# Optimization experiments

Hardware: AMD Instinct MI355X
Metric: run time of the kernel (lower is better)

The kernel has to match this reference:

```python
import jax, jax.numpy as jnp
import numpy as np
import math

B, L, C = 1, 4096, 1024
H = 16
D = C // H  # head_dim = 64


def setup_inputs() -> dict:
    key = jax.random.key(0)
    ks = jax.random.split(key, 5)
    s = 1.0 / math.sqrt(C)
    return {
        "x": jax.random.normal(ks[0], (B, L, C), dtype=jnp.float32),
        "Wq": jax.random.normal(ks[1], (C, C), dtype=jnp.float32) * s,
        "Wk": jax.random.normal(ks[2], (C, C), dtype=jnp.float32) * s,
        "Wv": jax.random.normal(ks[3], (C, C), dtype=jnp.float32) * s,
        "Wo": jax.random.normal(ks[4], (C, C), dtype=jnp.float32) * s,
    }


def reference(x, Wq, Wk, Wv, Wo):
    # Projections (bias=False). Wq etc. are applied as x @ W (equivalent
    # parameterization to torch Linear's x @ W.T with transposed storage).
    q = (x @ Wq).reshape(B, L, H, D).transpose(0, 2, 1, 3)  # (B,H,L,D)
    k = (x @ Wk).reshape(B, L, H, D).transpose(0, 2, 1, 3)
    v = (x @ Wv).reshape(B, L, H, D).transpose(0, 2, 1, 3)

    scale = 1.0 / math.sqrt(D)
    scores = jnp.einsum("bhqd,bhkd->bhqk", q, k) * scale  # (B,H,L,L)
    causal = jnp.tril(jnp.ones((L, L), dtype=bool))
    scores = jnp.where(causal[None, None, :, :], scores, -jnp.inf)
    probs = jax.nn.softmax(scores, axis=-1)  # dropout p=0 -> identity

    out = jnp.einsum("bhqk,bhkd->bhqd", probs, v)  # (B,H,L,D)
    out = out.transpose(0, 2, 1, 3).reshape(B, L, C)
    return out @ Wo  # resid dropout p=0 -> identity
```

## Files before the change

### kernel.cpp

```cpp
#include <hip/hip_runtime.h>

#define L_SEQ 4096
#define C_DIM 1024
#define H_NUM 16
#define D_HEAD 64
#define LDQKV 3072

typedef __bf16 bf16x8 __attribute__((ext_vector_type(8)));
typedef __bf16 bf16x4 __attribute__((ext_vector_type(4)));
typedef float f32x4 __attribute__((ext_vector_type(4)));
typedef float f32x16 __attribute__((ext_vector_type(16)));
typedef unsigned int u32;
typedef u32 u32x4 __attribute__((ext_vector_type(4)));

#define AS1 __attribute__((address_space(1)))
#define AS3 __attribute__((address_space(3)))

#define SC_LOG2E 0.1803368801111204f

__device__ inline __bf16 f2bf(float f) {
  unsigned u = __builtin_bit_cast(unsigned, f);
  u = (u + 0x7fffu + ((u >> 16) & 1u)) >> 16;
  unsigned short s = (unsigned short)u;
  return __builtin_bit_cast(__bf16, s);
}

__device__ inline void gload_lds16(const __bf16* g, __bf16* l) {
  __builtin_amdgcn_global_load_lds((const AS1 void*)g, (AS3 void*)l, 16, 0, 0);
}

__global__ __launch_bounds__(256) void cvt_f32_bf16(const float* __restrict__ in,
                                                    __bf16* __restrict__ out) {
  int i = (blockIdx.x * 256 + threadIdx.x) * 4;
  float4 v = *(const float4*)(in + i);
  bf16x4 o = {f2bf(v.x), f2bf(v.y), f2bf(v.z), f2bf(v.w)};
  *(bf16x4*)(out + i) = o;
}

__global__ __launch_bounds__(256) void transpose_cvt4(const float* __restrict__ W0,
                                                      const float* __restrict__ W1,
                                                      const float* __restrict__ W2,
                                                      const float* __restrict__ W3,
                                                      __bf16* __restrict__ dst) {
  __shared__ float t[32][33];
  const int z = blockIdx.z;
  const float* W = (z == 0) ? W0 : (z == 1) ? W1 : (z == 2) ? W2 : W3;
  __bf16* Wt = dst + (size_t)z * 1048576;
  const int tx = threadIdx.x, ty = threadIdx.y;
  const int c0 = blockIdx.x * 32, r0 = blockIdx.y * 32;
#pragma unroll
  for (int k = 0; k < 4; ++k)
    t[ty + k * 8][tx] = W[(size_t)(r0 + ty + k * 8) * C_DIM + c0 + tx];
  __syncthreads();
#pragma unroll
  for (int k = 0; k < 4; ++k)
    Wt[(size_t)(c0 + ty + k * 8) * C_DIM + r0 + tx] = f2bf(t[tx][ty + k * 8]);
}

__global__ __launch_bounds__(256) void transpose_v(const __bf16* __restrict__ QKV,
                                                   __bf16* __restrict__ Vt) {
  __shared__ __bf16 t[32][34];
  const int tx = threadIdx.x, ty = threadIdx.y;
  const int q0 = blockIdx.x * 32, c0 = blockIdx.y * 32;
#pragma unroll
  for (int k = 0; k < 4; ++k)
    t[ty + k * 8][tx] = QKV[(size_t)(q0 + ty + k * 8) * LDQKV + 2048 + c0 + tx];
  __syncthreads();
#pragma unroll
  for (int k = 0; k < 4; ++k)
    Vt[(size_t)(c0 + ty + k * 8) * L_SEQ + q0 + tx] = t[tx][ty + k * 8];
}

template <bool OUT_BF16>
__global__ __launch_bounds__(256) void gemm_bt(const __bf16* __restrict__ A,
                                               const __bf16* __restrict__ Bt,
                                               void* __restrict__ Cp,
                                               int M, int N, int K,
                                               float cscale, int scale_ncols) {
  __shared__ __bf16 As[128 * 32];
  __shared__ __bf16 Bs[128 * 32];
  const int tid = threadIdx.x;
  const int lane = tid & 63;
  const int wave = tid >> 6;
  const int wm = wave >> 1, wn = wave & 1;
  const int c16 = lane & 15, g4 = lane >> 4;
  const int srow = lane >> 2, scol = (lane & 3) * 8;

  f32x4 acc[4][4] = {};

  const size_t arow0 = (size_t)blockIdx.x * 128;
  const size_t brow0 = (size_t)blockIdx.y * 128;

  for (int kt = 0; kt < K; kt += 32) {
#pragma unroll
    for (int i = 0; i < 2; ++i) {
      const int row = i * 64 + wave * 16 + srow;
      gload_lds16(A + (arow0 + row) * K + kt + scol, As + (i * 64 + wave * 16) * 32);
      gload_lds16(Bt + (brow0 + row) * K + kt + scol, Bs + (i * 64 + wave * 16) * 32);
    }
    __syncthreads();
    bf16x8 af[4], bfr[4];
#pragma unroll
    for (int mi = 0; mi < 4; ++mi)
      af[mi] = *(const bf16x8*)(As + (wm * 64 + mi * 16 + c16) * 32 + g4 * 8);
#pragma unroll
    for (int ni = 0; ni < 4; ++ni)
      bfr[ni] = *(const bf16x8*)(Bs + (wn * 64 + ni * 16 + c16) * 32 + g4 * 8);
#pragma unroll
    for (int mi = 0; mi < 4; ++mi)
#pragma unroll
      for (int ni = 0; ni < 4; ++ni)
        acc[mi][ni] = __builtin_amdgcn_mfma_f32_16x16x32_bf16(af[mi], bfr[ni], acc[mi][ni], 0, 0, 0);
    __syncthreads();
  }

  const float esc = ((int)brow0 < scale_ncols) ? cscale : 1.0f;
#pragma unroll
  for (int mi = 0; mi < 4; ++mi)
#pragma unroll
    for (int ni = 0; ni < 4; ++ni)
#pragma unroll
      for (int i = 0; i < 4; ++i) {
        size_t row = arow0 + wm * 64 + mi * 16 + g4 * 4 + i;
        size_t col = brow0 + wn * 64 + ni * 16 + c16;
        if (OUT_BF16)
          ((__bf16*)Cp)[row * N + col] = f2bf(acc[mi][ni][i] * esc);
        else
          ((float*)Cp)[row * N + col] = acc[mi][ni][i];
      }
}

__global__ __launch_bounds__(256, 2) void attn_fwd(const __bf16* __restrict__ Q,
                                                   const __bf16* __restrict__ Kg,
                                                   const __bf16* __restrict__ Vt,
                                                   __bf16* __restrict__ O) {
  const int bid = blockIdx.x;
  const int h = bid & 15;
  const int qt = 31 - (bid >> 4);
  const int nt = 2 * qt + 2;

  __shared__ __bf16 Ks[2][64 * 64];
  __shared__ __bf16 Vs[2][64 * 64];

  const int tid = threadIdx.x;
  const int lane = tid & 63;
  const int wave = tid >> 6;
  const int l31 = lane & 31;
  const int hl = lane >> 5;
  const int qbase = qt * 128 + wave * 32;
  const int q = qbase + l31;
  const int kvmax_w = (qbase + 31) >> 6;

  const int rl = lane >> 3;
  const int cs = (lane & 7) ^ rl;

  auto stage = [&](int kv, int b) {
#pragma unroll
    for (int i = 0; i < 2; ++i) {
      const int r = (i * 4 + wave) * 8 + rl;
      gload_lds16(Kg + (size_t)(kv * 64 + r) * LDQKV + h * D_HEAD + cs * 8,
                  &Ks[b][(i * 4 + wave) * 512]);
      gload_lds16(Vt + (size_t)(h * D_HEAD + r) * L_SEQ + kv * 64 + cs * 8,
                  &Vs[b][(i * 4 + wave) * 512]);
    }
  };

  stage(0, 0);

  bf16x8 qf[4];
  {
    const __bf16* qp = Q + (size_t)q * LDQKV + h * D_HEAD + hl * 8;
#pragma unroll
    for (int s = 0; s < 4; ++s) qf[s] = *(const bf16x8*)(qp + s * 16);
  }

  f32x16 acc0 = {}, acc1 = {};
  float m = -1e30f, lsum = 0.f;

  int cur = 0;
  for (int kv = 0; kv < nt; ++kv) {
    if (kv + 1 < nt) {
      stage(kv + 1, cur ^ 1);
      asm volatile("s_waitcnt vmcnt(4)" ::: "memory");
    } else {
      asm volatile("s_waitcnt vmcnt(0)" ::: "memory");
    }
    __builtin_amdgcn_sched_barrier(0);
    __builtin_amdgcn_s_barrier();
    __builtin_amdgcn_sched_barrier(0);

    if (kv <= kvmax_w) {
      char* const KsB = (char*)&Ks[cur][0];
      char* const VsB = (char*)&Vs[cur][0];

      f32x16 st0 = {}, st1 = {};
      __builtin_amdgcn_s_setprio(1);
#pragma unroll
      for (int s = 0; s < 4; ++s) {
        const int ch = s * 2 + hl;
        bf16x8 a0 = *(const bf16x8*)(KsB + l31 * 128 + ((ch ^ (l31 & 7)) << 4));
        bf16x8 a1 = *(const bf16x8*)(KsB + (32 + l31) * 128 + ((ch ^ (l31 & 7)) << 4));
        st0 = __builtin_amdgcn_mfma_f32_32x32x16_bf16(a0, qf[s], st0, 0, 0, 0);
        st1 = __builtin_amdgcn_mfma_f32_32x32x16_bf16(a1, qf[s], st1, 0, 0, 0);
      }
      __builtin_amdgcn_s_setprio(0);

      if (kv == kvmax_w) {
#pragma unroll
        for (int r = 0; r < 16; ++r) {
          const int kr = (r & 3) + 8 * (r >> 2) + 4 * hl;
          const int k0 = kv * 64 + kr;
          st0[r] = (k0 <= q) ? st0[r] : -1e30f;
          st1[r] = (k0 + 32 <= q) ? st1[r] : -1e30f;
        }
      }

      float t[16];
#pragma unroll
      for (int r = 0; r < 16; ++r) t[r] = fmaxf(st0[r], st1[r]);
#pragma unroll
      for (int w = 8; w > 0; w >>= 1)
#pragma unroll
        for (int r = 0; r < w; ++r) t[r] = fmaxf(t[r], t[r + w]);
      float mx = fmaxf(t[0], __shfl_xor(t[0], 32, 64));
      const float mnew = fmaxf(m, mx);
      const float corr = exp2f(m - mnew);
      m = mnew;

#pragma unroll
      for (int r = 0; r < 16; ++r) {
        st0[r] = exp2f(st0[r] - m);
        st1[r] = exp2f(st1[r] - m);
      }
      float sm[16];
#pragma unroll
      for (int r = 0; r < 16; ++r) sm[r] = st0[r] + st1[r];
#pragma unroll
      for (int w = 8; w > 0; w >>= 1)
#pragma unroll
        for (int r = 0; r < w; ++r) sm[r] = sm[r] + sm[r + w];
      float sl = sm[0] + __shfl_xor(sm[0], 32, 64);
      lsum = lsum * corr + sl;
      acc0 *= corr;
      acc1 *= corr;

      u32 w0[8], w1[8];
#pragma unroll
      for (int i = 0; i < 8; ++i) {
        asm("v_cvt_pk_bf16_f32 %0, %1, %2" : "=v"(w0[i]) : "v"(st0[2 * i]), "v"(st0[2 * i + 1]));
        asm("v_cvt_pk_bf16_f32 %0, %1, %2" : "=v"(w1[i]) : "v"(st1[2 * i]), "v"(st1[2 * i + 1]));
      }
      u32 e0a = (u32)__shfl_xor((int)(hl ? w0[0] : w0[2]), 32, 64);
      u32 e0b = (u32)__shfl_xor((int)(hl ? w0[1] : w0[3]), 32, 64);
      u32 e0c = (u32)__shfl_xor((int)(hl ? w0[4] : w0[6]), 32, 64);
      u32 e0d = (u32)__shfl_xor((int)(hl ? w0[5] : w0[7]), 32, 64);
      u32 e1a = (u32)__shfl_xor((int)(hl ? w1[0] : w1[2]), 32, 64);
      u32 e1b = (u32)__shfl_xor((int)(hl ? w1[1] : w1[3]), 32, 64);
      u32 e1c = (u32)__shfl_xor((int)(hl ? w1[4] : w1[6]), 32, 64);
      u32 e1d = (u32)__shfl_xor((int)(hl ? w1[5] : w1[7]), 32, 64);
      u32x4 f0 = hl ? (u32x4){e0a, e0b, w0[2], w0[3]} : (u32x4){w0[0], w0[1], e0a, e0b};
      u32x4 f1 = hl ? (u32x4){e0c, e0d, w0[6], w0[7]} : (u32x4){w0[4], w0[5], e0c, e0d};
      u32x4 f2 = hl ? (u32x4){e1a, e1b, w1[2], w1[3]} : (u32x4){w1[0], w1[1], e1a, e1b};
      u32x4 f3 = hl ? (u32x4){e1c, e1d, w1[6], w1[7]} : (u32x4){w1[4], w1[5], e1c, e1d};
      bf16x8 pb0 = __builtin_bit_cast(bf16x8, f0);
      bf16x8 pb1 = __builtin_bit_cast(bf16x8, f1);
      bf16x8 pb2 = __builtin_bit_cast(bf16x8, f2);
      bf16x8 pb3 = __builtin_bit_cast(bf16x8, f3);

      __builtin_amdgcn_s_setprio(1);
#pragma unroll
      for (int s = 0; s < 4; ++s) {
        const bf16x8 pb = (s == 0) ? pb0 : (s == 1) ? pb1 : (s == 2) ? pb2 : pb3;
        const int ch = s * 2 + hl;
        bf16x8 va0 = *(const bf16x8*)(VsB + l31 * 128 + ((ch ^ (l31 & 7)) << 4));
        bf16x8 va1 = *(const bf16x8*)(VsB + (32 + l31) * 128 + ((ch ^ (l31 & 7)) << 4));
        acc0 = __builtin_amdgcn_mfma_f32_32x32x16_bf16(va0, pb, acc0, 0, 0, 0);
        acc1 = __builtin_amdgcn_mfma_f32_32x32x16_bf16(va1, pb, acc1, 0, 0, 0);
      }
      __builtin_amdgcn_s_setprio(0);
    }

    __builtin_amdgcn_sched_barrier(0);
    __builtin_amdgcn_s_barrier();
    __builtin_amdgcn_sched_barrier(0);
    cur ^= 1;
  }

  const float rinv = 1.0f / lsum;
  char* const Po = (char*)&Ks[0][0] + wave * 4096;
#pragma unroll
  for (int dt = 0; dt < 2; ++dt) {
#pragma unroll
    for (int i = 0; i < 8; ++i) {
      const int r = 2 * i;
      const int d = dt * 32 + (r & 3) + 8 * (r >> 2) + 4 * hl;
      float lo = (dt ? acc1[r] : acc0[r]) * rinv;
      float hi = (dt ? acc1[r + 1] : acc0[r + 1]) * rinv;
      u32 wv;
      asm("v_cvt_pk_bf16_f32 %0, %1, %2" : "=v"(wv) : "v"(lo), "v"(hi));
      *(u32*)(Po + l31 * 128 + (((d >> 3) ^ (l31 & 7)) << 4) + (d & 7) * 2) = wv;
    }
  }
  asm volatile("s_waitcnt lgkmcnt(0)" ::: "memory");
  __builtin_amdgcn_sched_barrier(0);
#pragma unroll
  for (int j = 0; j < 4; ++j) {
    const int qr = lane >> 1;
    const int c = (lane & 1) * 4 + j;
    bf16x8 ov = *(const bf16x8*)(Po + qr * 128 + ((c ^ (qr & 7)) << 4));
    *(bf16x8*)(O + (size_t)(qbase + qr) * C_DIM + h * D_HEAD + c * 8) = ov;
  }
}

extern "C" void kernel_launch(void* const* d_in, const int* in_sizes, int n_in,
                              void* d_out, int out_size, void* d_ws, size_t ws_size,
                              hipStream_t stream) {
  const float* x = (const float*)d_in[0];
  const float* Wq = (const float*)d_in[1];
  const float* Wk = (const float*)d_in[2];
  const float* Wv = (const float*)d_in[3];
  const float* Wo = (const float*)d_in[4];
  float* out = (float*)d_out;

  char* ws = (char*)d_ws;
  __bf16* xb    = (__bf16*)(ws);
  __bf16* WqkvT = (__bf16*)(ws + (8u << 20));
  __bf16* QKVb  = (__bf16*)(ws + (16u << 20));
  __bf16* Vtb   = (__bf16*)(ws + (40u << 20));
  __bf16* WoT   = WqkvT + (size_t)3 * 1048576;
  __bf16* Ab    = xb;

  cvt_f32_bf16<<<4096, 256, 0, stream>>>(x, xb);

  transpose_cvt4<<<dim3(32, 32, 4), dim3(32, 8), 0, stream>>>(Wq, Wk, Wv, Wo, WqkvT);

  gemm_bt<true><<<dim3(L_SEQ / 128, LDQKV / 128), 256, 0, stream>>>(
      xb, WqkvT, QKVb, L_SEQ, LDQKV, C_DIM, SC_LOG2E, 1024);

  transpose_v<<<dim3(L_SEQ / 32, C_DIM / 32), dim3(32, 8), 0, stream>>>(QKVb, Vtb);

  attn_fwd<<<512, 256, 0, stream>>>(QKVb, QKVb + 1024, Vtb, Ab);

  gemm_bt<false><<<dim3(L_SEQ / 128, C_DIM / 128), 256, 0, stream>>>(
      Ab, WoT, out, L_SEQ, C_DIM, C_DIM, 1.0f, 0);
}
```

Before: 258.6 us.

## Pair complementary causal query tiles per block for balanced attention work

The attention kernel now gives each block two 64-row query tiles, p and 63-p, processed back to back so every block runs exactly 65 KV iterations. This replaces 128-row tiles with uneven causal work and per-wave idle iterations, removing load imbalance and wasted barrier trips. Blocks shrink to 128 threads (2 waves), each wave staging more loads, and a separate LDS buffer holds the first tile's epilogue output. The risk is lower per-block parallelism and more K/V traffic, since each 64-row tile reloads K/V independently.

```diff
diff --git a/kernel.cpp b/kernel.cpp
--- a/kernel.cpp
+++ b/kernel.cpp
@@ -130,58 +130,86 @@
       }
 }
 
-__global__ __launch_bounds__(256, 2) void attn_fwd(const __bf16* __restrict__ Q,
+__global__ __launch_bounds__(128, 2) void attn_fwd(const __bf16* __restrict__ Q,
                                                    const __bf16* __restrict__ Kg,
                                                    const __bf16* __restrict__ Vt,
                                                    __bf16* __restrict__ O) {
   const int bid = blockIdx.x;
   const int h = bid & 15;
-  const int qt = 31 - (bid >> 4);
-  const int nt = 2 * qt + 2;
+  const int p = bid >> 4;
+  const int nA = 64 - p;
+  const int NT = 65;
 
   __shared__ __bf16 Ks[2][64 * 64];
   __shared__ __bf16 Vs[2][64 * 64];
+  __shared__ __bf16 PoS[2][2048];
 
   const int tid = threadIdx.x;
   const int lane = tid & 63;
   const int wave = tid >> 6;
   const int l31 = lane & 31;
   const int hl = lane >> 5;
-  const int qbase = qt * 128 + wave * 32;
-  const int q = qbase + l31;
-  const int kvmax_w = (qbase + 31) >> 6;
-
   const int rl = lane >> 3;
   const int cs = (lane & 7) ^ rl;
+  const int thr = wave * 32 + l31;
 
   auto stage = [&](int kv, int b) {
 #pragma unroll
-    for (int i = 0; i < 2; ++i) {
-      const int r = (i * 4 + wave) * 8 + rl;
+    for (int i = 0; i < 4; ++i) {
+      const int r = (i * 2 + wave) * 8 + rl;
       gload_lds16(Kg + (size_t)(kv * 64 + r) * LDQKV + h * D_HEAD + cs * 8,
-                  &Ks[b][(i * 4 + wave) * 512]);
+                  &Ks[b][(i * 2 + wave) * 512]);
       gload_lds16(Vt + (size_t)(h * D_HEAD + r) * L_SEQ + kv * 64 + cs * 8,
-                  &Vs[b][(i * 4 + wave) * 512]);
+                  &Vs[b][(i * 2 + wave) * 512]);
     }
   };
 
   stage(0, 0);
 
+  int qbase = (nA - 1) * 64 + wave * 32;
   bf16x8 qf[4];
   {
-    const __bf16* qp = Q + (size_t)q * LDQKV + h * D_HEAD + hl * 8;
+    const __bf16* qp = Q + (size_t)(qbase + l31) * LDQKV + h * D_HEAD + hl * 8;
 #pragma unroll
     for (int s = 0; s < 4; ++s) qf[s] = *(const bf16x8*)(qp + s * 16);
   }
 
   f32x16 acc0 = {}, acc1 = {};
   float m = -1e30f, lsum = 0.f;
-
   int cur = 0;
-  for (int kv = 0; kv < nt; ++kv) {
-    if (kv + 1 < nt) {
-      stage(kv + 1, cur ^ 1);
-      asm volatile("s_waitcnt vmcnt(4)" ::: "memory");
+
+  auto epilogue = [&](int qb) {
+    const float rinv = 1.0f / lsum;
+    char* const Po = (char*)&PoS[wave][0];
+#pragma unroll
+    for (int dt = 0; dt < 2; ++dt) {
+#pragma unroll
+      for (int i = 0; i < 8; ++i) {
+        const int r = 2 * i;
+        const int d = dt * 32 + (r & 3) + 8 * (r >> 2) + 4 * hl;
+        float lo = (dt ? acc1[r] : acc0[r]) * rinv;
+        float hi = (dt ? acc1[r + 1] : acc0[r + 1]) * rinv;
+        u32 wv;
+        asm("v_cvt_pk_bf16_f32 %0, %1, %2" : "=v"(wv) : "v"(lo), "v"(hi));
+        *(u32*)(Po + l31 * 128 + (((d >> 3) ^ (l31 & 7)) << 4) + (d & 7) * 2) = wv;
+      }
+    }
+    asm volatile("s_waitcnt lgkmcnt(0)" ::: "memory");
+    __builtin_amdgcn_sched_barrier(0);
+#pragma unroll
+    for (int j = 0; j < 4; ++j) {
+      const int qr = lane >> 1;
+      const int c = (lane & 1) * 4 + j;
+      bf16x8 ov = *(const bf16x8*)(Po + qr * 128 + ((c ^ (qr & 7)) << 4));
+      *(bf16x8*)(O + (size_t)(qb + qr) * C_DIM + h * D_HEAD + c * 8) = ov;
+    }
+  };
+
+  for (int it = 0; it < NT; ++it) {
+    if (it + 1 < NT) {
+      const int kvn = (it + 1 < nA) ? it + 1 : it + 1 - nA;
+      stage(kvn, cur ^ 1);
+      asm volatile("s_waitcnt vmcnt(8)" ::: "memory");
     } else {
       asm volatile("s_waitcnt vmcnt(0)" ::: "memory");
     }
@@ -189,127 +217,114 @@
     __builtin_amdgcn_s_barrier();
     __builtin_amdgcn_sched_barrier(0);
 
-    if (kv <= kvmax_w) {
-      char* const KsB = (char*)&Ks[cur][0];
-      char* const VsB = (char*)&Vs[cur][0];
-
-      f32x16 st0 = {}, st1 = {};
-      __builtin_amdgcn_s_setprio(1);
-#pragma unroll
-      for (int s = 0; s < 4; ++s) {
-        const int ch = s * 2 + hl;
-        bf16x8 a0 = *(const bf16x8*)(KsB + l31 * 128 + ((ch ^ (l31 & 7)) << 4));
-        bf16x8 a1 = *(const bf16x8*)(KsB + (32 + l31) * 128 + ((ch ^ (l31 & 7)) << 4));
-        st0 = __builtin_amdgcn_mfma_f32_32x32x16_bf16(a0, qf[s], st0, 0, 0, 0);
-        st1 = __builtin_amdgcn_mfma_f32_32x32x16_bf16(a1, qf[s], st1, 0, 0, 0);
+    char* const KsB = (char*)&Ks[cur][0];
+    char* const VsB = (char*)&Vs[cur][0];
+    const bool diag = (it == nA - 1) || (it == NT - 1);
+
+    f32x16 st0 = {}, st1 = {};
+    __builtin_amdgcn_s_setprio(1);
+#pragma unroll
+    for (int s = 0; s < 4; ++s) {
+      const int ch = s * 2 + hl;
+      bf16x8 a0 = *(const bf16x8*)(KsB + l31 * 128 + ((ch ^ (l31 & 7)) << 4));
+      bf16x8 a1 = *(const bf16x8*)(KsB + (32 + l31) * 128 + ((ch ^ (l31 & 7)) << 4));
+      st0 = __builtin_amdgcn_mfma_f32_32x32x16_bf16(a0, qf[s], st0, 0, 0, 0);
+      st1 = __builtin_amdgcn_mfma_f32_32x32x16_bf16(a1, qf[s], st1, 0, 0, 0);
+    }
+    __builtin_amdgcn_s_setprio(0);
+
+    if (diag) {
+#pragma unroll
+      for (int r = 0; r < 16; ++r) {
+        const int kr = (r & 3) + 8 * (r >> 2) + 4 * hl;
+        st0[r] = (kr <= thr) ? st0[r] : -1e30f;
+        st1[r] = (kr + 32 <= thr) ? st1[r] : -1e30f;
       }
-      __builtin_amdgcn_s_setprio(0);
-
-      if (kv == kvmax_w) {
-#pragma unroll
-        for (int r = 0; r < 16; ++r) {
-          const int kr = (r & 3) + 8 * (r >> 2) + 4 * hl;
-          const int k0 = kv * 64 + kr;
-          st0[r] = (k0 <= q) ? st0[r] : -1e30f;
-          st1[r] = (k0 + 32 <= q) ? st1[r] : -1e30f;
-        }
-      }
-
-      float t[16];
-#pragma unroll
-      for (int r = 0; r < 16; ++r) t[r] = fmaxf(st0[r], st1[r]);
-#pragma unroll
-      for (int w = 8; w > 0; w >>= 1)
-#pragma unroll
-        for (int r = 0; r < w; ++r) t[r] = fmaxf(t[r], t[r + w]);
-      float mx = fmaxf(t[0], __shfl_xor(t[0], 32, 64));
-      const float mnew = fmaxf(m, mx);
-      const float corr = exp2f(m - mnew);
-      m = mnew;
-
-#pragma unroll
-      for (int r = 0; r < 16; ++r) {
-        st0[r] = exp2f(st0[r] - m);
-        st1[r] = exp2f(st1[r] - m);
-      }
-      float sm[16];
-#pragma unroll
-      for (int r = 0; r < 16; ++r) sm[r] = st0[r] + st1[r];
-#pragma unroll
-      for (int w = 8; w > 0; w >>= 1)
-#pragma unroll
-        for (int r = 0; r < w; ++r) sm[r] = sm[r] + sm[r + w];
-      float sl = sm[0] + __shfl_xor(sm[0], 32, 64);
-      lsum = lsum * corr + sl;
-      acc0 *= corr;
-      acc1 *= corr;
-
-      u32 w0[8], w1[8];
-#pragma unroll
-      for (int i = 0; i < 8; ++i) {
-        asm("v_cvt_pk_bf16_f32 %0, %1, %2" : "=v"(w0[i]) : "v"(st0[2 * i]), "v"(st0[2 * i + 1]));
-        asm("v_cvt_pk_bf16_f32 %0, %1, %2" : "=v"(w1[i]) : "v"(st1[2 * i]), "v"(st1[2 * i + 1]));
-      }
-      u32 e0a = (u32)__shfl_xor((int)(hl ? w0[0] : w0[2]), 32, 64);
-      u32 e0b = (u32)__shfl_xor((int)(hl ? w0[1] : w0[3]), 32, 64);
-      u32 e0c = (u32)__shfl_xor((int)(hl ? w0[4] : w0[6]), 32, 64);
-      u32 e0d = (u32)__shfl_xor((int)(hl ? w0[5] : w0[7]), 32, 64);
-      u32 e1a = (u32)__shfl_xor((int)(hl ? w1[0] : w1[2]), 32, 64);
-      u32 e1b = (u32)__shfl_xor((int)(hl ? w1[1] : w1[3]), 32, 64);
-      u32 e1c = (u32)__shfl_xor((int)(hl ? w1[4] : w1[6]), 32, 64);
-      u32 e1d = (u32)__shfl_xor((int)(hl ? w1[5] : w1[7]), 32, 64);
-      u32x4 f0 = hl ? (u32x4){e0a, e0b, w0[2], w0[3]} : (u32x4){w0[0], w0[1], e0a, e0b};
-      u32x4 f1 = hl ? (u32x4){e0c, e0d, w0[6], w0[7]} : (u32x4){w0[4], w0[5], e0c, e0d};
-      u32x4 f2 = hl ? (u32x4){e1a, e1b, w1[2], w1[3]} : (u32x4){w1[0], w1[1], e1a, e1b};
-      u32x4 f3 = hl ? (u32x4){e1c, e1d, w1[6], w1[7]} : (u32x4){w1[4], w1[5], e1c, e1d};
-      bf16x8 pb0 = __builtin_bit_cast(bf16x8, f0);
-      bf16x8 pb1 = __builtin_bit_cast(bf16x8, f1);
-      bf16x8 pb2 = __builtin_bit_cast(bf16x8, f2);
-      bf16x8 pb3 = __builtin_bit_cast(bf16x8, f3);
-
-      __builtin_amdgcn_s_setprio(1);
-#pragma unroll
-      for (int s = 0; s < 4; ++s) {
-        const bf16x8 pb = (s == 0) ? pb0 : (s == 1) ? pb1 : (s == 2) ? pb2 : pb3;
-        const int ch = s * 2 + hl;
-        bf16x8 va0 = *(const bf16x8*)(VsB + l31 * 128 + ((ch ^ (l31 & 7)) << 4));
-        bf16x8 va1 = *(const bf16x8*)(VsB + (32 + l31) * 128 + ((ch ^ (l31 & 7)) << 4));
-        acc0 = __builtin_amdgcn_mfma_f32_32x32x16_bf16(va0, pb, acc0, 0, 0, 0);
-        acc1 = __builtin_amdgcn_mfma_f32_32x32x16_bf16(va1, pb, acc1, 0, 0, 0);
-      }
-      __builtin_amdgcn_s_setprio(0);
-    }
+    }
+
+    float t[16];
+#pragma unroll
+    for (int r = 0; r < 16; ++r) t[r] = fmaxf(st0[r], st1[r]);
+#pragma unroll
+    for (int w = 8; w > 0; w >>= 1)
+#pragma unroll
+      for (int r = 0; r < w; ++r) t[r] = fmaxf(t[r], t[r + w]);
+    float mx = fmaxf(t[0], __shfl_xor(t[0], 32, 64));
+    const float mnew = fmaxf(m, mx);
+    const float corr = exp2f(m - mnew);
+    m = mnew;
+
+#pragma unroll
+    for (int r = 0; r < 16; ++r) {
+      st0[r] = exp2f(st0[r] - m);
+      st1[r] = exp2f(st1[r] - m);
+    }
+    float sm[16];
+#pragma unroll
+    for (int r = 0; r < 16; ++r) sm[r] = st0[r] + st1[r];
+#pragma unroll
+    for (int w = 8; w > 0; w >>= 1)
+#pragma unroll
+      for (int r = 0; r < w; ++r) sm[r] = sm[r] + sm[r + w];
+    float sl = sm[0] + __shfl_xor(sm[0], 32, 64);
+    lsum = lsum * corr + sl;
+    acc0 *= corr;
+    acc1 *= corr;
+
+    u32 w0[8], w1[8];
+#pragma unroll
+    for (int i = 0; i < 8; ++i) {
+      asm("v_cvt_pk_bf16_f32 %0, %1, %2" : "=v"(w0[i]) : "v"(st0[2 * i]), "v"(st0[2 * i + 1]));
+      asm("v_cvt_pk_bf16_f32 %0, %1, %2" : "=v"(w1[i]) : "v"(st1[2 * i]), "v"(st1[2 * i + 1]));
+    }
+    u32 e0a = (u32)__shfl_xor((int)(hl ? w0[0] : w0[2]), 32, 64);
+    u32 e0b = (u32)__shfl_xor((int)(hl ? w0[1] : w0[3]), 32, 64);
+    u32 e0c = (u32)__shfl_xor((int)(hl ? w0[4] : w0[6]), 32, 64);
+    u32 e0d = (u32)__shfl_xor((int)(hl ? w0[5] : w0[7]), 32, 64);
+    u32 e1a = (u32)__shfl_xor((int)(hl ? w1[0] : w1[2]), 32, 64);
+    u32 e1b = (u32)__shfl_xor((int)(hl ? w1[1] : w1[3]), 32, 64);
+    u32 e1c = (u32)__shfl_xor((int)(hl ? w1[4] : w1[6]), 32, 64);
+    u32 e1d = (u32)__shfl_xor((int)(hl ? w1[5] : w1[7]), 32, 64);
+    u32x4 f0 = hl ? (u32x4){e0a, e0b, w0[2], w0[3]} : (u32x4){w0[0], w0[1], e0a, e0b};
+    u32x4 f1 = hl ? (u32x4){e0c, e0d, w0[6], w0[7]} : (u32x4){w0[4], w0[5], e0c, e0d};
+    u32x4 f2 = hl ? (u32x4){e1a, e1b, w1[2], w1[3]} : (u32x4){w1[0], w1[1], e1a, e1b};
+    u32x4 f3 = hl ? (u32x4){e1c, e1d, w1[6], w1[7]} : (u32x4){w1[4], w1[5], e1c, e1d};
+    bf16x8 pb0 = __builtin_bit_cast(bf16x8, f0);
+    bf16x8 pb1 = __builtin_bit_cast(bf16x8, f1);
+    bf16x8 pb2 = __builtin_bit_cast(bf16x8, f2);
+    bf16x8 pb3 = __builtin_bit_cast(bf16x8, f3);
+
+    __builtin_amdgcn_s_setprio(1);
+#pragma unroll
+    for (int s = 0; s < 4; ++s) {
+      const bf16x8 pb = (s == 0) ? pb0 : (s == 1) ? pb1 : (s == 2) ? pb2 : pb3;
+      const int ch = s * 2 + hl;
+      bf16x8 va0 = *(const bf16x8*)(VsB + l31 * 128 + ((ch ^ (l31 & 7)) << 4));
+      bf16x8 va1 = *(const bf16x8*)(VsB + (32 + l31) * 128 + ((ch ^ (l31 & 7)) << 4));
+      acc0 = __builtin_amdgcn_mfma_f32_32x32x16_bf16(va0, pb, acc0, 0, 0, 0);
+      acc1 = __builtin_amdgcn_mfma_f32_32x32x16_bf16(va1, pb, acc1, 0, 0, 0);
+    }
+    __builtin_amdgcn_s_setprio(0);
 
     __builtin_amdgcn_sched_barrier(0);
     __builtin_amdgcn_s_barrier();
     __builtin_amdgcn_sched_barrier(0);
     cur ^= 1;
+
+    if (it == nA - 1) {
+      epilogue(qbase);
+      qbase = p * 64 + wave * 32;
+      const __bf16* qp = Q + (size_t)(qbase + l31) * LDQKV + h * D_HEAD + hl * 8;
+#pragma unroll
+      for (int s = 0; s < 4; ++s) qf[s] = *(const bf16x8*)(qp + s * 16);
+      acc0 = (f32x16){};
+      acc1 = (f32x16){};
+      m = -1e30f;
+      lsum = 0.f;
+    }
   }
 
-  const float rinv = 1.0f / lsum;
-  char* const Po = (char*)&Ks[0][0] + wave * 4096;
-#pragma unroll
-  for (int dt = 0; dt < 2; ++dt) {
-#pragma unroll
-    for (int i = 0; i < 8; ++i) {
-      const int r = 2 * i;
-      const int d = dt * 32 + (r & 3) + 8 * (r >> 2) + 4 * hl;
-      float lo = (dt ? acc1[r] : acc0[r]) * rinv;
-      float hi = (dt ? acc1[r + 1] : acc0[r + 1]) * rinv;
-      u32 wv;
-      asm("v_cvt_pk_bf16_f32 %0, %1, %2" : "=v"(wv) : "v"(lo), "v"(hi));
-      *(u32*)(Po + l31 * 128 + (((d >> 3) ^ (l31 & 7)) << 4) + (d & 7) * 2) = wv;
-    }
-  }
-  asm volatile("s_waitcnt lgkmcnt(0)" ::: "memory");
-  __builtin_amdgcn_sched_barrier(0);
-#pragma unroll
-  for (int j = 0; j < 4; ++j) {
-    const int qr = lane >> 1;
-    const int c = (lane & 1) * 4 + j;
-    bf16x8 ov = *(const bf16x8*)(Po + qr * 128 + ((c ^ (qr & 7)) << 4));
-    *(bf16x8*)(O + (size_t)(qbase + qr) * C_DIM + h * D_HEAD + c * 8) = ov;
-  }
+  epilogue(qbase);
 }
 
 extern "C" void kernel_launch(void* const* d_in, const int* in_sizes, int n_in,
@@ -339,7 +354,7 @@
 
   transpose_v<<<dim3(L_SEQ / 32, C_DIM / 32), dim3(32, 8), 0, stream>>>(QKVb, Vtb);
 
-  attn_fwd<<<512, 256, 0, stream>>>(QKVb, QKVb + 1024, Vtb, Ab);
+  attn_fwd<<<512, 128, 0, stream>>>(QKVb, QKVb + 1024, Vtb, Ab);
 
   gemm_bt<false><<<dim3(L_SEQ / 128, C_DIM / 128), 256, 0, stream>>>(
       Ab, WoT, out, L_SEQ, C_DIM, C_DIM, 1.0f, 0);
```

Measured after the change: 293.4 us. 13.5% more time.

## Compute V transposed directly via swapped GEMM and rebalance causal attention blocks

Applied to the files above, without the earlier changes.

The fused QKV projection is split into a QK GEMM and a separate GEMM that computes V^T as Wv^T @ x^T, so V comes out already transposed and the transpose_v kernel with its extra read/write pass over V goes away. The attention block-to-tile mapping also changes so the first half of the blocks run long causal tiles in descending order and the second half run short tiles ascending, which is meant to even out work across waves of blocks. This adds one extra kernel launch and a GEMM with a different shape (M=1024, N=4096).

```diff
diff --git a/kernel.cpp b/kernel.cpp
--- a/kernel.cpp
+++ b/kernel.cpp
@@ -4,7 +4,7 @@
 #define C_DIM 1024
 #define H_NUM 16
 #define D_HEAD 64
-#define LDQKV 3072
+#define LDQK 2048
 
 typedef __bf16 bf16x8 __attribute__((ext_vector_type(8)));
 typedef __bf16 bf16x4 __attribute__((ext_vector_type(4)));
@@ -55,20 +55,6 @@
 #pragma unroll
   for (int k = 0; k < 4; ++k)
     Wt[(size_t)(c0 + ty + k * 8) * C_DIM + r0 + tx] = f2bf(t[tx][ty + k * 8]);
-}
-
-__global__ __launch_bounds__(256) void transpose_v(const __bf16* __restrict__ QKV,
-                                                   __bf16* __restrict__ Vt) {
-  __shared__ __bf16 t[32][34];
-  const int tx = threadIdx.x, ty = threadIdx.y;
-  const int q0 = blockIdx.x * 32, c0 = blockIdx.y * 32;
-#pragma unroll
-  for (int k = 0; k < 4; ++k)
-    t[ty + k * 8][tx] = QKV[(size_t)(q0 + ty + k * 8) * LDQKV + 2048 + c0 + tx];
-  __syncthreads();
-#pragma unroll
-  for (int k = 0; k < 4; ++k)
-    Vt[(size_t)(c0 + ty + k * 8) * L_SEQ + q0 + tx] = t[tx][ty + k * 8];
 }
 
 template <bool OUT_BF16>
@@ -136,7 +122,8 @@
                                                    __bf16* __restrict__ O) {
   const int bid = blockIdx.x;
   const int h = bid & 15;
-  const int qt = 31 - (bid >> 4);
+  const int g = (bid >> 4) & 15;
+  const int qt = (bid < 256) ? (31 - g) : g;
   const int nt = 2 * qt + 2;
 
   __shared__ __bf16 Ks[2][64 * 64];
@@ -158,7 +145,7 @@
 #pragma unroll
     for (int i = 0; i < 2; ++i) {
       const int r = (i * 4 + wave) * 8 + rl;
-      gload_lds16(Kg + (size_t)(kv * 64 + r) * LDQKV + h * D_HEAD + cs * 8,
+      gload_lds16(Kg + (size_t)(kv * 64 + r) * LDQK + h * D_HEAD + cs * 8,
                   &Ks[b][(i * 4 + wave) * 512]);
       gload_lds16(Vt + (size_t)(h * D_HEAD + r) * L_SEQ + kv * 64 + cs * 8,
                   &Vs[b][(i * 4 + wave) * 512]);
@@ -169,7 +156,7 @@
 
   bf16x8 qf[4];
   {
-    const __bf16* qp = Q + (size_t)q * LDQKV + h * D_HEAD + hl * 8;
+    const __bf16* qp = Q + (size_t)q * LDQK + h * D_HEAD + hl * 8;
 #pragma unroll
     for (int s = 0; s < 4; ++s) qf[s] = *(const bf16x8*)(qp + s * 16);
   }
@@ -325,8 +312,9 @@
   char* ws = (char*)d_ws;
   __bf16* xb    = (__bf16*)(ws);
   __bf16* WqkvT = (__bf16*)(ws + (8u << 20));
-  __bf16* QKVb  = (__bf16*)(ws + (16u << 20));
-  __bf16* Vtb   = (__bf16*)(ws + (40u << 20));
+  __bf16* QKb   = (__bf16*)(ws + (16u << 20));
+  __bf16* Vtb   = (__bf16*)(ws + (32u << 20));
+  __bf16* WvT   = WqkvT + (size_t)2 * 1048576;
   __bf16* WoT   = WqkvT + (size_t)3 * 1048576;
   __bf16* Ab    = xb;
 
@@ -334,13 +322,14 @@
 
   transpose_cvt4<<<dim3(32, 32, 4), dim3(32, 8), 0, stream>>>(Wq, Wk, Wv, Wo, WqkvT);
 
-  gemm_bt<true><<<dim3(L_SEQ / 128, LDQKV / 128), 256, 0, stream>>>(
-      xb, WqkvT, QKVb, L_SEQ, LDQKV, C_DIM, SC_LOG2E, 1024);
-
-  transpose_v<<<dim3(L_SEQ / 32, C_DIM / 32), dim3(32, 8), 0, stream>>>(QKVb, Vtb);
-
-  attn_fwd<<<512, 256, 0, stream>>>(QKVb, QKVb + 1024, Vtb, Ab);
-
-  gemm_bt<false><<<dim3(L_SEQ / 128, C_DIM / 128), 256, 0, stream>>>(
+  gemm_bt<true><<<dim3(32, 16), 256, 0, stream>>>(
+      xb, WqkvT, QKb, L_SEQ, LDQK, C_DIM, SC_LOG2E, 1024);
+
+  gemm_bt<true><<<dim3(8, 32), 256, 0, stream>>>(
+      WvT, xb, Vtb, C_DIM, L_SEQ, C_DIM, 1.0f, 0);
+
+  attn_fwd<<<512, 256, 0, stream>>>(QKb, QKb + 1024, Vtb, Ab);
+
+  gemm_bt<false><<<dim3(32, 8), 256, 0, stream>>>(
       Ab, WoT, out, L_SEQ, C_DIM, C_DIM, 1.0f, 0);
 }
```

After: 278.1 us. 1.08x slower.
